# Optimization experiments

Hardware: AMD Instinct MI355X
Metric: run time of the kernel (lower is better)

The kernel has to match this reference:

```python
import jax, jax.numpy as jnp
import numpy as np

# Dimensions (match init_kwargs / input_specs)
N, C_IN, C, H, W = 2, 256, 256, 80, 80
G, KS = 16, 3                 # groups, kernel_size
K = KS * KS                   # sampling points per group
CG = C // G                   # channels per group
PAD, STRIDE, DIL = 1, 1, 1
OFFSET_SCALE = 1.0
EPS = 1e-5                    # BatchNorm2d eps (eval mode)


def setup_inputs() -> dict:
    key = jax.random.key(0)
    ks = jax.random.split(key, 12)
    rn = lambda k, shape, s=0.02: jax.random.normal(k, shape, dtype=jnp.float32) * s
    return {
        "x": jax.random.normal(ks[0], (N, C_IN, H, W), dtype=jnp.float32),
        # Conv(inc, ouc, k=1): 1x1 conv (bias=False) + BN + SiLU
        "w1": rn(ks[1], (C_IN, C)),
        "bn1_g": jnp.ones((C,), jnp.float32), "bn1_b": jnp.zeros((C,), jnp.float32),
        "bn1_m": rn(ks[2], (C,), 0.1),
        "bn1_v": jax.random.uniform(ks[3], (C,), minval=0.5, maxval=1.5, dtype=jnp.float32),
        # DCNv4: value_proj, fused offset_mask, output_proj
        "wv": rn(ks[4], (C, C)), "bv": jnp.zeros((C,), jnp.float32),
        "wom": rn(ks[5], (C, G * K * 3)), "bom": rn(ks[6], (G * K * 3,), 0.1),
        "wo": rn(ks[7], (C, C)), "bo": jnp.zeros((C,), jnp.float32),
        # trailing BatchNorm2d + SiLU
        "bn2_g": jnp.ones((C,), jnp.float32), "bn2_b": jnp.zeros((C,), jnp.float32),
        "bn2_m": rn(ks[8], (C,), 0.1),
        "bn2_v": jax.random.uniform(ks[9], (C,), minval=0.5, maxval=1.5, dtype=jnp.float32),
    }


def _bn(x, g, b, m, v):
    # eval-mode BatchNorm over last (channel) axis
    return (x - m) * jax.lax.rsqrt(v + EPS) * g + b


def _forward(x, w1, bn1_g, bn1_b, bn1_m, bn1_v, wv, bv, wom, bom, wo, bo,
             bn2_g, bn2_b, bn2_m, bn2_v):
    # --- Conv 1x1 + BN + SiLU (channels-last) ---
    h = jnp.einsum('nchw,cd->nhwd', x, w1)                 # (N,H,W,C)
    h = jax.nn.silu(_bn(h, bn1_g, bn1_b, bn1_m, bn1_v))

    # --- DCNv4 ---
    xf = h.reshape(N, H * W, C)
    value = (xf @ wv + bv).reshape(N, H, W, G, CG)         # value projection
    om = (xf @ wom + bom).reshape(N, H, W, G, 3 * K)       # fused offset+mask
    offset = om[..., :2 * K].reshape(N, H, W, G, K, 2) * OFFSET_SCALE  # (x,y) pairs
    mask = om[..., 2 * K:]                                 # (N,H,W,G,K); v4: no softmax

    # sampling pixel coords: p = out_pos*stride - pad + kernel_offset*dil + learned offset
    ky, kx = jnp.meshgrid(jnp.arange(KS), jnp.arange(KS), indexing='ij')
    ky = (ky.reshape(-1) * DIL).astype(jnp.float32)        # (K,)
    kx = (kx.reshape(-1) * DIL).astype(jnp.float32)
    base_y = (jnp.arange(H) * STRIDE - PAD).astype(jnp.float32)
    base_x = (jnp.arange(W) * STRIDE - PAD).astype(jnp.float32)
    py = base_y[None, :, None, None, None] + ky[None, None, None, None, :] + offset[..., 1]
    px = base_x[None, None, :, None, None] + kx[None, None, None, None, :] + offset[..., 0]

    y0 = jnp.floor(py); x0 = jnp.floor(px)
    wy = py - y0;       wx = px - x0
    y0i = y0.astype(jnp.int32); x0i = x0.astype(jnp.int32)
    y1i = y0i + 1;             x1i = x0i + 1

    ni = jnp.arange(N)[:, None, None, None, None]
    gi = jnp.arange(G)[None, None, None, :, None]

    def gather(yi, xi):
        valid = ((yi >= 0) & (yi < H) & (xi >= 0) & (xi < W)).astype(value.dtype)
        v = value[ni, jnp.clip(yi, 0, H - 1), jnp.clip(xi, 0, W - 1), gi]  # (N,H,W,G,K,CG)
        return v, valid

    acc = jnp.zeros((N, H, W, G, CG), dtype=value.dtype)
    for yi, xi, wgt in ((y0i, x0i, (1 - wy) * (1 - wx)),
                        (y0i, x1i, (1 - wy) * wx),
                        (y1i, x0i, wy * (1 - wx)),
                        (y1i, x1i, wy * wx)):
        v, valid = gather(yi, xi)
        acc = acc + jnp.einsum('nhwgk,nhwgkc->nhwgc', mask * wgt * valid, v)

    out = acc.reshape(N, H * W, C) @ wo + bo               # output projection
    out = out.reshape(N, H, W, C)

    # --- BN + SiLU (wrapper tail) ---
    out = jax.nn.silu(_bn(out, bn2_g, bn2_b, bn2_m, bn2_v))
    return jnp.transpose(out, (0, 3, 1, 2))                # (N,C,H,W)


def reference(x, w1, bn1_g, bn1_b, bn1_m, bn1_v, wv, bv, wom, bom, wo, bo,
              bn2_g, bn2_b, bn2_m, bn2_v):
    return _forward(x, w1, bn1_g, bn1_b, bn1_m, bn1_v, wv, bv, wom, bom,
                    wo, bo, bn2_g, bn2_b, bn2_m, bn2_v)
```

## Files before the change

kernel.cpp:

```cpp
#include <hip/hip_runtime.h>
#include <hip/hip_bf16.h>
#include <math.h>

typedef __attribute__((ext_vector_type(8))) short bf16x8;
typedef __attribute__((ext_vector_type(4))) float f32x4;

#define NB   2
#define CC   256
#define HH   80
#define WW   80
#define HWSZ 6400
#define MM   (NB * HWSZ)
#define NCAT 768
#define EPSB 1e-5f

__device__ inline void t32g(const float* __restrict__ in, int inld, int scol0,
                            int ncols, __hip_bfloat16* __restrict__ out,
                            int orow0, int r0, int tid)
{
    __shared__ float tile[32][33];
    int tx = tid & 31, ty = tid >> 5;
#pragma unroll
    for (int i = 0; i < 32; i += 8)
        tile[ty + i][tx] = (tx < ncols)
            ? in[(size_t)(r0 + ty + i) * inld + scol0 + tx] : 0.f;
    __syncthreads();
#pragma unroll
    for (int i = 0; i < 32; i += 8)
        out[(size_t)(orow0 + ty + i) * 256 + r0 + tx] =
            __float2bfloat16(tile[tx][ty + i]);
}

__global__ __launch_bounds__(256) void prep_all_k(
    const float* __restrict__ x,
    const float* __restrict__ w1, const float* __restrict__ wv,
    const float* __restrict__ wom, const float* __restrict__ wo,
    const float* __restrict__ bv, const float* __restrict__ bom,
    __hip_bfloat16* __restrict__ xT,
    __hip_bfloat16* __restrict__ w1T, __hip_bfloat16* __restrict__ BcatT,
    __hip_bfloat16* __restrict__ woT, float* __restrict__ bcat)
{
    int b = blockIdx.x, t = threadIdx.x;
    if (b < 3200) {
        __shared__ float tile[32][33];
        int z = b / 1600, r = b % 1600;
        int by = r / 200, bx = r % 200;
        const float* inz = x + (size_t)256 * HWSZ * z;
        __hip_bfloat16* outz = xT + (size_t)HWSZ * 256 * z;
        int bc = bx * 32, br = by * 32;
        int tx = t & 31, ty = t >> 5;
#pragma unroll
        for (int i = 0; i < 32; i += 8)
            tile[ty + i][tx] = inz[(size_t)(br + ty + i) * HWSZ + bc + tx];
        __syncthreads();
#pragma unroll
        for (int i = 0; i < 32; i += 8)
            outz[(size_t)(bc + ty + i) * 256 + br + tx] =
                __float2bfloat16(tile[tx][ty + i]);
        return;
    }
    b -= 3200;
    if (b < 64) {
        t32g(w1, 256, (b >> 3) * 32, 32, w1T, (b >> 3) * 32, (b & 7) * 32, t);
    } else if (b < 128) {
        int b2 = b - 64;
        t32g(wv, 256, (b2 >> 3) * 32, 32, BcatT, (b2 >> 3) * 32, (b2 & 7) * 32, t);
    } else if (b < 192) {
        int b2 = b - 128;
        t32g(wo, 256, (b2 >> 3) * 32, 32, woT, (b2 >> 3) * 32, (b2 & 7) * 32, t);
    } else if (b < 320) {
        int b2 = b - 192;
        int g = b2 >> 3, ct = b2 & 7;
        t32g(wom, 432, g * 27, 27, BcatT + 256 * 256, g * 32, ct * 32, t);
    } else {
        bcat[t] = bv[t];
#pragma unroll
        for (int j = 0; j < 2; ++j) {
            int r = j * 256 + t;
            int g = r >> 5, jj = r & 31;
            bcat[256 + r] = (jj < 27) ? bom[g * 27 + jj] : 0.f;
        }
    }
}

template <int EPI>
__global__ __launch_bounds__(256) void gemm_mfma(
    const short* __restrict__ A, const short* __restrict__ Bt,
    const float* __restrict__ bias,
    const float* __restrict__ bng, const float* __restrict__ bnb,
    const float* __restrict__ bnm, const float* __restrict__ bnv,
    void* __restrict__ Cout, int ldC)
{
    __shared__ __align__(16) char smem[49152];
    short* As = (short*)smem;
    short* Bs = (short*)(smem + 16384);

    const int t = threadIdx.x;
    const int w = t >> 6, l = t & 63;
    const int wr = w >> 1, wc = w & 1;
    const int m0 = blockIdx.x * 64, n0 = blockIdx.y * 128;

    f32x4 acc[2][4] = {};

    auto STAGE = [&](int b, int k0) {
        short* AsB = As + b * 4096;
        short* BsB = Bs + b * 8192;
#pragma unroll
        for (int i = 0; i < 2; ++i) {
            int s = (w << 1) + i;
            int c = (s << 6) + l;
            int row = c >> 3, ch = c & 7;
            const short* ga = A + (size_t)(m0 + row) * 256 + k0 + (ch << 3);
            __builtin_amdgcn_global_load_lds(
                (const __attribute__((address_space(1))) void*)ga,
                (__attribute__((address_space(3))) void*)(AsB + (s << 9)), 16, 0, 0);
        }
#pragma unroll
        for (int i = 0; i < 4; ++i) {
            int s = (w << 2) + i;
            int c = (s << 6) + l;
            int row = c >> 3, ch = c & 7;
            const short* gb = Bt + (size_t)(n0 + row) * 256 + k0 + (ch << 3);
            __builtin_amdgcn_global_load_lds(
                (const __attribute__((address_space(1))) void*)gb,
                (__attribute__((address_space(3))) void*)(BsB + (s << 9)), 16, 0, 0);
        }
    };

    auto COMPUTE = [&](int b) {
        const short* AsB = As + b * 4096;
        const short* BsB = Bs + b * 8192;
#pragma unroll
        for (int kk = 0; kk < 2; ++kk) {
            bf16x8 af[2], bfr[4];
#pragma unroll
            for (int mi = 0; mi < 2; ++mi)
                af[mi] = *(const bf16x8*)(AsB + (wr * 32 + mi * 16 + (l & 15)) * 64 +
                                          kk * 32 + ((l >> 4) << 3));
#pragma unroll
            for (int ni = 0; ni < 4; ++ni)
                bfr[ni] = *(const bf16x8*)(BsB + (wc * 64 + ni * 16 + (l & 15)) * 64 +
                                           kk * 32 + ((l >> 4) << 3));
#pragma unroll
            for (int mi = 0; mi < 2; ++mi)
#pragma unroll
                for (int ni = 0; ni < 4; ++ni)
                    acc[mi][ni] = __builtin_amdgcn_mfma_f32_16x16x32_bf16(
                        af[mi], bfr[ni], acc[mi][ni], 0, 0, 0);
        }
    };

    STAGE(0, 0);
    __syncthreads();
#pragma unroll
    for (int tt = 0; tt < 4; ++tt) {
        if (tt < 3) STAGE((tt + 1) & 1, (tt + 1) * 64);
        COMPUTE(tt & 1);
        __syncthreads();
    }

    if (EPI == 0) {
#pragma unroll
        for (int ni = 0; ni < 4; ++ni) {
            int chn = n0 + wc * 64 + ni * 16 + (l & 15);
            float bb = bias[chn];
#pragma unroll
            for (int mi = 0; mi < 2; ++mi) {
                int mbase = m0 + wr * 32 + mi * 16 + ((l >> 4) << 2);
#pragma unroll
                for (int j = 0; j < 4; ++j) {
                    float v = acc[mi][ni][j] + bb;
                    ((__hip_bfloat16*)Cout)[(size_t)(mbase + j) * ldC + chn] =
                        __float2bfloat16(v);
                }
            }
        }
    } else {
#pragma unroll
        for (int ni = 0; ni < 4; ++ni) {
            int chn = n0 + wc * 64 + ni * 16 + (l & 15);
            float mu = bnm[chn], iv = rsqrtf(bnv[chn] + EPSB);
            float gm = bng[chn], bt = bnb[chn];
#pragma unroll
            for (int mi = 0; mi < 2; ++mi) {
                int mbase = m0 + wr * 32 + mi * 16 + ((l >> 4) << 2);
#pragma unroll
                for (int j = 0; j < 4; ++j) {
                    float v = acc[mi][ni][j];
                    v = (v - mu) * iv * gm + bt;
                    v = v / (1.f + __expf(-v));
                    ((__hip_bfloat16*)Cout)[(size_t)(mbase + j) * ldC + chn] =
                        __float2bfloat16(v);
                }
            }
        }
    }
}

__global__ __launch_bounds__(512) void gemm3_fused_k(
    const __hip_bfloat16* __restrict__ C2, const short* __restrict__ woT,
    const float* __restrict__ bias,
    const float* __restrict__ bng, const float* __restrict__ bnb,
    const float* __restrict__ bnm, const float* __restrict__ bnv,
    float* __restrict__ out)
{
    __shared__ __align__(16) char smem[98304];
    short* As = (short*)smem;
    short* Bs = (short*)(smem + 32768);

    const int t = threadIdx.x;
    const int w = t >> 6, l = t & 63;
    const int wr = w >> 2, wc = w & 3;
    const int m0 = blockIdx.x * 64;
    const int nimg = m0 / HWSZ;
    const int p0 = m0 % HWSZ;

    auto STAGE_B = [&](int b, int k0) {
        short* BsB = Bs + b * 16384;
#pragma unroll
        for (int i = 0; i < 4; ++i) {
            int c = t + i * 512;
            int row = c >> 3, ch = c & 7;
            const short* gb = woT + (size_t)row * 256 + k0 + (ch << 3);
            __builtin_amdgcn_global_load_lds(
                (const __attribute__((address_space(1))) void*)gb,
                (__attribute__((address_space(3))) void*)(BsB + ((w << 6) + (i << 9)) * 8),
                16, 0, 0);
        }
    };

    STAGE_B(0, 0);

#pragma unroll
    for (int it = 0; it < 2; ++it) {
        int task = it * 512 + t;
        int g = task & 15, px = task >> 4;
        int mp = m0 + px;
        int p = mp % HWSZ;
        int y = p / WW, x = p % WW;

        const unsigned* omw =
            (const unsigned*)(C2 + (size_t)mp * NCAT + 256 + g * 32);
        const __hip_bfloat16* vb = C2 + (size_t)nimg * HWSZ * NCAT + g * 16;

        float mk[9];
        {
            unsigned mw[5];
#pragma unroll
            for (int i = 0; i < 5; ++i) mw[i] = omw[9 + i];
#pragma unroll
            for (int i = 0; i < 9; ++i) {
                unsigned w16 = (i & 1) ? (mw[i >> 1] >> 16) : (mw[i >> 1] & 0xffffu);
                union { unsigned u; float f; } cv; cv.u = w16 << 16;
                mk[i] = cv.f;
            }
        }

        float acc[16] = {};
#pragma unroll
        for (int k = 0; k < 9; ++k) {
            unsigned ow = omw[k];
            union { unsigned u; float f; } cx, cy;
            cx.u = (ow & 0xffffu) << 16;
            cy.u = ow & 0xffff0000u;
            float px_ = (float)(x - 1 + (k % 3)) + cx.f;
            float py_ = (float)(y - 1 + (k / 3)) + cy.f;
            float fx = floorf(px_), fy = floorf(py_);
            float wx = px_ - fx, wy = py_ - fy;
            int x0 = (int)fx, y0 = (int)fy;
            int x1 = x0 + 1, y1 = y0 + 1;
            float ax0 = ((unsigned)x0 < (unsigned)WW) ? (1.f - wx) : 0.f;
            float ax1 = ((unsigned)x1 < (unsigned)WW) ? wx : 0.f;
            float ay0 = ((unsigned)y0 < (unsigned)HH) ? mk[k] * (1.f - wy) : 0.f;
            float ay1 = ((unsigned)y1 < (unsigned)HH) ? mk[k] * wy : 0.f;
            int xc0 = min(max(x0, 0), WW - 1);
            int xc1 = min(max(x1, 0), WW - 1);
            int yc0 = min(max(y0, 0), HH - 1);
            int yc1 = min(max(y1, 0), HH - 1);
            const __hip_bfloat16* r0 = vb + (size_t)(yc0 * WW) * NCAT;
            const __hip_bfloat16* r1 = vb + (size_t)(yc1 * WW) * NCAT;
            const __hip_bfloat16* pts[4] = {
                r0 + (size_t)xc0 * NCAT, r0 + (size_t)xc1 * NCAT,
                r1 + (size_t)xc0 * NCAT, r1 + (size_t)xc1 * NCAT };
            float wgt[4] = { ay0 * ax0, ay0 * ax1, ay1 * ax0, ay1 * ax1 };
#pragma unroll
            for (int q = 0; q < 4; ++q) {
                bf16x8 v0 = *(const bf16x8*)pts[q];
                bf16x8 v1 = *(const bf16x8*)(pts[q] + 8);
#pragma unroll
                for (int j = 0; j < 8; ++j) {
                    union { unsigned u; float f; } cv;
                    cv.u = ((unsigned)(unsigned short)v0[j]) << 16;
                    acc[j] = fmaf(wgt[q], cv.f, acc[j]);
                }
#pragma unroll
                for (int j = 0; j < 8; ++j) {
                    union { unsigned u; float f; } cv;
                    cv.u = ((unsigned)(unsigned short)v1[j]) << 16;
                    acc[8 + j] = fmaf(wgt[q], cv.f, acc[8 + j]);
                }
            }
        }

        bf16x8 ov0, ov1;
#pragma unroll
        for (int j = 0; j < 8; ++j) {
            __hip_bfloat16 b0 = __float2bfloat16(acc[j]);
            __hip_bfloat16 b1 = __float2bfloat16(acc[8 + j]);
            ov0[j] = *reinterpret_cast<short*>(&b0);
            ov1[j] = *reinterpret_cast<short*>(&b1);
        }
        *(bf16x8*)(As + px * 256 + g * 16) = ov0;
        *(bf16x8*)(As + px * 256 + g * 16 + 8) = ov1;
    }
    __syncthreads();

    f32x4 acc[2][4] = {};
#pragma unroll
    for (int tt = 0; tt < 4; ++tt) {
        if (tt < 3) STAGE_B((tt + 1) & 1, (tt + 1) * 64);
        const short* BsB = Bs + (tt & 1) * 16384;
        const int k0 = tt * 64;
#pragma unroll
        for (int kk = 0; kk < 2; ++kk) {
            bf16x8 af[2], bfr[4];
#pragma unroll
            for (int mi = 0; mi < 2; ++mi)
                af[mi] = *(const bf16x8*)(As + (wr * 32 + mi * 16 + (l & 15)) * 256 +
                                          k0 + kk * 32 + ((l >> 4) << 3));
#pragma unroll
            for (int ni = 0; ni < 4; ++ni)
                bfr[ni] = *(const bf16x8*)(BsB + (wc * 64 + ni * 16 + (l & 15)) * 64 +
                                           kk * 32 + ((l >> 4) << 3));
#pragma unroll
            for (int mi = 0; mi < 2; ++mi)
#pragma unroll
                for (int ni = 0; ni < 4; ++ni)
                    acc[mi][ni] = __builtin_amdgcn_mfma_f32_16x16x32_bf16(
                        af[mi], bfr[ni], acc[mi][ni], 0, 0, 0);
        }
        __syncthreads();
    }

    float(*CtT)[68] = (float(*)[68])smem;
#pragma unroll
    for (int h2 = 0; h2 < 4; ++h2) {
        if (wc == h2) {
#pragma unroll
            for (int ni = 0; ni < 4; ++ni)
#pragma unroll
                for (int mi = 0; mi < 2; ++mi)
#pragma unroll
                    for (int j = 0; j < 4; ++j)
                        CtT[ni * 16 + (l & 15)]
                           [wr * 32 + mi * 16 + ((l >> 4) << 2) + j] =
                               acc[mi][ni][j];
        }
        __syncthreads();
#pragma unroll
        for (int it = 0; it < 2; ++it) {
            int e4 = it * 512 + t;
            int row = e4 >> 4;
            int c4 = e4 & 15;
            int chn = h2 * 64 + row;
            float bb = bias[chn];
            float mu = bnm[chn], iv = rsqrtf(bnv[chn] + EPSB);
            float gm = bng[chn], bt = bnb[chn];
            f32x4 v = *(f32x4*)&CtT[row][c4 * 4];
#pragma unroll
            for (int j = 0; j < 4; ++j) {
                float u = v[j] + bb;
                u = (u - mu) * iv * gm + bt;
                u = u / (1.f + __expf(-u));
                v[j] = u;
            }
            *(f32x4*)&out[(size_t)(nimg * CC + chn) * HWSZ + p0 + c4 * 4] = v;
        }
        __syncthreads();
    }
}

extern "C" void kernel_launch(void* const* d_in, const int* in_sizes, int n_in,
                              void* d_out, int out_size, void* d_ws, size_t ws_size,
                              hipStream_t stream)
{
    const float* x    = (const float*)d_in[0];
    const float* w1   = (const float*)d_in[1];
    const float* bn1g = (const float*)d_in[2];
    const float* bn1b = (const float*)d_in[3];
    const float* bn1m = (const float*)d_in[4];
    const float* bn1v = (const float*)d_in[5];
    const float* wv   = (const float*)d_in[6];
    const float* bv   = (const float*)d_in[7];
    const float* wom  = (const float*)d_in[8];
    const float* bom  = (const float*)d_in[9];
    const float* wo   = (const float*)d_in[10];
    const float* bo   = (const float*)d_in[11];
    const float* bn2g = (const float*)d_in[12];
    const float* bn2b = (const float*)d_in[13];
    const float* bn2m = (const float*)d_in[14];
    const float* bn2v = (const float*)d_in[15];
    float* out = (float*)d_out;

    char* w = (char*)d_ws;
    __hip_bfloat16* xT    = (__hip_bfloat16*)(w);
    __hip_bfloat16* hbuf  = (__hip_bfloat16*)(w + 6553600);
    __hip_bfloat16* C2    = (__hip_bfloat16*)(w + 13107200);
    __hip_bfloat16* w1T   = (__hip_bfloat16*)(w + 39321600);
    __hip_bfloat16* woT   = (__hip_bfloat16*)(w + 39452672);
    __hip_bfloat16* BcatT = (__hip_bfloat16*)(w + 39583744);
    float*          bcat  = (float*)(w + 39976960);

    dim3 blk(256);

    prep_all_k<<<dim3(3521), blk, 0, stream>>>(
        x, w1, wv, wom, wo, bv, bom, xT, w1T, BcatT, woT, bcat);

    gemm_mfma<1><<<dim3(200, 2), blk, 0, stream>>>(
        (const short*)xT, (const short*)w1T, nullptr,
        bn1g, bn1b, bn1m, bn1v, hbuf, CC);

    gemm_mfma<0><<<dim3(200, 6), blk, 0, stream>>>(
        (const short*)hbuf, (const short*)BcatT, bcat,
        nullptr, nullptr, nullptr, nullptr, C2, NCAT);

    gemm3_fused_k<<<dim3(200), dim3(512), 0, stream>>>(
        C2, (const short*)woT, bo, bn2g, bn2b, bn2m, bn2v, out);
}
```

Baseline: 148.9 us.

## Fuse all stages into one persistent kernel with grid barriers

Replaces the four separate launches (prep transpose, two GEMMs, fused deformable-sample+output GEMM) with one persistent kernel of 256 blocks of 512 threads, separated by atomic-counter grid barriers. The GEMM tiles are widened to 64x256 with 8 waves. The aim is to remove launch gaps and tail effects between stages. In exchange, only 256 blocks run each stage: 200 tiles in GEMM1 and phase 3 leave some CUs idle, and 600 tiles in GEMM2 need three uneven waves. It also adds spin-wait barrier overhead, a memset per call, and deadlock risk if not all 256 blocks are co-resident.

```diff
diff --git a/kernel.cpp b/kernel.cpp
--- a/kernel.cpp
+++ b/kernel.cpp
@@ -13,123 +13,63 @@
 #define MM   (NB * HWSZ)
 #define NCAT 768
 #define EPSB 1e-5f
-
-__device__ inline void t32g(const float* __restrict__ in, int inld, int scol0,
-                            int ncols, __hip_bfloat16* __restrict__ out,
-                            int orow0, int r0, int tid)
+#define NBLK 256
+
+__device__ __forceinline__ void gridbar(unsigned* cnt)
 {
-    __shared__ float tile[32][33];
-    int tx = tid & 31, ty = tid >> 5;
-#pragma unroll
-    for (int i = 0; i < 32; i += 8)
-        tile[ty + i][tx] = (tx < ncols)
-            ? in[(size_t)(r0 + ty + i) * inld + scol0 + tx] : 0.f;
     __syncthreads();
-#pragma unroll
-    for (int i = 0; i < 32; i += 8)
-        out[(size_t)(orow0 + ty + i) * 256 + r0 + tx] =
-            __float2bfloat16(tile[tx][ty + i]);
+    if (threadIdx.x == 0) {
+        __threadfence();
+        __hip_atomic_fetch_add(cnt, 1u, __ATOMIC_ACQ_REL, __HIP_MEMORY_SCOPE_AGENT);
+        while (__hip_atomic_load(cnt, __ATOMIC_ACQUIRE, __HIP_MEMORY_SCOPE_AGENT) < (unsigned)NBLK) {}
+        __threadfence();
+    }
+    __syncthreads();
 }
 
-__global__ __launch_bounds__(256) void prep_all_k(
-    const float* __restrict__ x,
-    const float* __restrict__ w1, const float* __restrict__ wv,
-    const float* __restrict__ wom, const float* __restrict__ wo,
-    const float* __restrict__ bv, const float* __restrict__ bom,
-    __hip_bfloat16* __restrict__ xT,
-    __hip_bfloat16* __restrict__ w1T, __hip_bfloat16* __restrict__ BcatT,
-    __hip_bfloat16* __restrict__ woT, float* __restrict__ bcat)
-{
-    int b = blockIdx.x, t = threadIdx.x;
-    if (b < 3200) {
-        __shared__ float tile[32][33];
-        int z = b / 1600, r = b % 1600;
-        int by = r / 200, bx = r % 200;
-        const float* inz = x + (size_t)256 * HWSZ * z;
-        __hip_bfloat16* outz = xT + (size_t)HWSZ * 256 * z;
-        int bc = bx * 32, br = by * 32;
-        int tx = t & 31, ty = t >> 5;
-#pragma unroll
-        for (int i = 0; i < 32; i += 8)
-            tile[ty + i][tx] = inz[(size_t)(br + ty + i) * HWSZ + bc + tx];
-        __syncthreads();
-#pragma unroll
-        for (int i = 0; i < 32; i += 8)
-            outz[(size_t)(bc + ty + i) * 256 + br + tx] =
-                __float2bfloat16(tile[tx][ty + i]);
-        return;
-    }
-    b -= 3200;
-    if (b < 64) {
-        t32g(w1, 256, (b >> 3) * 32, 32, w1T, (b >> 3) * 32, (b & 7) * 32, t);
-    } else if (b < 128) {
-        int b2 = b - 64;
-        t32g(wv, 256, (b2 >> 3) * 32, 32, BcatT, (b2 >> 3) * 32, (b2 & 7) * 32, t);
-    } else if (b < 192) {
-        int b2 = b - 128;
-        t32g(wo, 256, (b2 >> 3) * 32, 32, woT, (b2 >> 3) * 32, (b2 & 7) * 32, t);
-    } else if (b < 320) {
-        int b2 = b - 192;
-        int g = b2 >> 3, ct = b2 & 7;
-        t32g(wom, 432, g * 27, 27, BcatT + 256 * 256, g * 32, ct * 32, t);
-    } else {
-        bcat[t] = bv[t];
-#pragma unroll
-        for (int j = 0; j < 2; ++j) {
-            int r = j * 256 + t;
-            int g = r >> 5, jj = r & 31;
-            bcat[256 + r] = (jj < 27) ? bom[g * 27 + jj] : 0.f;
-        }
-    }
-}
-
 template <int EPI>
-__global__ __launch_bounds__(256) void gemm_mfma(
+__device__ __forceinline__ void gemm64x256(
     const short* __restrict__ A, const short* __restrict__ Bt,
     const float* __restrict__ bias,
     const float* __restrict__ bng, const float* __restrict__ bnb,
     const float* __restrict__ bnm, const float* __restrict__ bnv,
-    void* __restrict__ Cout, int ldC)
+    __hip_bfloat16* __restrict__ Cout, int ldC, int m0, int n0,
+    char* smem, int t)
 {
-    __shared__ __align__(16) char smem[49152];
     short* As = (short*)smem;
     short* Bs = (short*)(smem + 16384);
-
-    const int t = threadIdx.x;
     const int w = t >> 6, l = t & 63;
-    const int wr = w >> 1, wc = w & 1;
-    const int m0 = blockIdx.x * 64, n0 = blockIdx.y * 128;
-
+    const int wr = w >> 2, wc = w & 3;
     f32x4 acc[2][4] = {};
 
     auto STAGE = [&](int b, int k0) {
         short* AsB = As + b * 4096;
-        short* BsB = Bs + b * 8192;
-#pragma unroll
-        for (int i = 0; i < 2; ++i) {
-            int s = (w << 1) + i;
-            int c = (s << 6) + l;
-            int row = c >> 3, ch = c & 7;
+        short* BsB = Bs + b * 16384;
+        {
+            int row = t >> 3, ch = t & 7;
             const short* ga = A + (size_t)(m0 + row) * 256 + k0 + (ch << 3);
             __builtin_amdgcn_global_load_lds(
                 (const __attribute__((address_space(1))) void*)ga,
-                (__attribute__((address_space(3))) void*)(AsB + (s << 9)), 16, 0, 0);
+                (__attribute__((address_space(3))) void*)(AsB + t * 8), 16, 0, 0);
         }
 #pragma unroll
         for (int i = 0; i < 4; ++i) {
-            int s = (w << 2) + i;
-            int c = (s << 6) + l;
+            int c = t + i * 512;
             int row = c >> 3, ch = c & 7;
             const short* gb = Bt + (size_t)(n0 + row) * 256 + k0 + (ch << 3);
             __builtin_amdgcn_global_load_lds(
                 (const __attribute__((address_space(1))) void*)gb,
-                (__attribute__((address_space(3))) void*)(BsB + (s << 9)), 16, 0, 0);
+                (__attribute__((address_space(3))) void*)(BsB + c * 8), 16, 0, 0);
         }
     };
 
-    auto COMPUTE = [&](int b) {
-        const short* AsB = As + b * 4096;
-        const short* BsB = Bs + b * 8192;
+    STAGE(0, 0);
+    __syncthreads();
+#pragma unroll
+    for (int tt = 0; tt < 4; ++tt) {
+        if (tt < 3) STAGE((tt + 1) & 1, (tt + 1) * 64);
+        const short* AsB = As + (tt & 1) * 4096;
+        const short* BsB = Bs + (tt & 1) * 16384;
 #pragma unroll
         for (int kk = 0; kk < 2; ++kk) {
             bf16x8 af[2], bfr[4];
@@ -148,70 +88,45 @@
                     acc[mi][ni] = __builtin_amdgcn_mfma_f32_16x16x32_bf16(
                         af[mi], bfr[ni], acc[mi][ni], 0, 0, 0);
         }
-    };
-
-    STAGE(0, 0);
-    __syncthreads();
-#pragma unroll
-    for (int tt = 0; tt < 4; ++tt) {
-        if (tt < 3) STAGE((tt + 1) & 1, (tt + 1) * 64);
-        COMPUTE(tt & 1);
         __syncthreads();
     }
 
-    if (EPI == 0) {
-#pragma unroll
-        for (int ni = 0; ni < 4; ++ni) {
-            int chn = n0 + wc * 64 + ni * 16 + (l & 15);
-            float bb = bias[chn];
-#pragma unroll
-            for (int mi = 0; mi < 2; ++mi) {
-                int mbase = m0 + wr * 32 + mi * 16 + ((l >> 4) << 2);
-#pragma unroll
-                for (int j = 0; j < 4; ++j) {
-                    float v = acc[mi][ni][j] + bb;
-                    ((__hip_bfloat16*)Cout)[(size_t)(mbase + j) * ldC + chn] =
-                        __float2bfloat16(v);
-                }
-            }
-        }
-    } else {
-#pragma unroll
-        for (int ni = 0; ni < 4; ++ni) {
-            int chn = n0 + wc * 64 + ni * 16 + (l & 15);
-            float mu = bnm[chn], iv = rsqrtf(bnv[chn] + EPSB);
-            float gm = bng[chn], bt = bnb[chn];
-#pragma unroll
-            for (int mi = 0; mi < 2; ++mi) {
-                int mbase = m0 + wr * 32 + mi * 16 + ((l >> 4) << 2);
-#pragma unroll
-                for (int j = 0; j < 4; ++j) {
-                    float v = acc[mi][ni][j];
-                    v = (v - mu) * iv * gm + bt;
+#pragma unroll
+    for (int ni = 0; ni < 4; ++ni) {
+        int chn = n0 + wc * 64 + ni * 16 + (l & 15);
+        float bb = (EPI == 0) ? bias[chn] : 0.f;
+        float mu = 0.f, iv = 0.f, gm = 0.f, bt2 = 0.f;
+        if (EPI == 1) {
+            mu = bnm[chn]; iv = rsqrtf(bnv[chn] + EPSB);
+            gm = bng[chn]; bt2 = bnb[chn];
+        }
+#pragma unroll
+        for (int mi = 0; mi < 2; ++mi) {
+            int mbase = m0 + wr * 32 + mi * 16 + ((l >> 4) << 2);
+#pragma unroll
+            for (int j = 0; j < 4; ++j) {
+                float v = acc[mi][ni][j] + bb;
+                if (EPI == 1) {
+                    v = (v - mu) * iv * gm + bt2;
                     v = v / (1.f + __expf(-v));
-                    ((__hip_bfloat16*)Cout)[(size_t)(mbase + j) * ldC + chn] =
-                        __float2bfloat16(v);
-                }
+                }
+                Cout[(size_t)(mbase + j) * ldC + chn] = __float2bfloat16(v);
             }
         }
     }
 }
 
-__global__ __launch_bounds__(512) void gemm3_fused_k(
+__device__ __forceinline__ void p3_fused(
     const __hip_bfloat16* __restrict__ C2, const short* __restrict__ woT,
     const float* __restrict__ bias,
     const float* __restrict__ bng, const float* __restrict__ bnb,
     const float* __restrict__ bnm, const float* __restrict__ bnv,
-    float* __restrict__ out)
+    float* __restrict__ out, int m0, char* smem, int t)
 {
-    __shared__ __align__(16) char smem[98304];
     short* As = (short*)smem;
     short* Bs = (short*)(smem + 32768);
-
-    const int t = threadIdx.x;
     const int w = t >> 6, l = t & 63;
     const int wr = w >> 2, wc = w & 3;
-    const int m0 = blockIdx.x * 64;
     const int nimg = m0 / HWSZ;
     const int p0 = m0 % HWSZ;
 
@@ -224,8 +139,7 @@
             const short* gb = woT + (size_t)row * 256 + k0 + (ch << 3);
             __builtin_amdgcn_global_load_lds(
                 (const __attribute__((address_space(1))) void*)gb,
-                (__attribute__((address_space(3))) void*)(BsB + ((w << 6) + (i << 9)) * 8),
-                16, 0, 0);
+                (__attribute__((address_space(3))) void*)(BsB + c * 8), 16, 0, 0);
         }
     };
 
@@ -365,12 +279,12 @@
             int chn = h2 * 64 + row;
             float bb = bias[chn];
             float mu = bnm[chn], iv = rsqrtf(bnv[chn] + EPSB);
-            float gm = bng[chn], bt = bnb[chn];
+            float gm = bng[chn], bt2 = bnb[chn];
             f32x4 v = *(f32x4*)&CtT[row][c4 * 4];
 #pragma unroll
             for (int j = 0; j < 4; ++j) {
                 float u = v[j] + bb;
-                u = (u - mu) * iv * gm + bt;
+                u = (u - mu) * iv * gm + bt2;
                 u = u / (1.f + __expf(-u));
                 v[j] = u;
             }
@@ -378,6 +292,104 @@
         }
         __syncthreads();
     }
+}
+
+__global__ __launch_bounds__(512) void mega_k(
+    const float* __restrict__ x, const float* __restrict__ w1,
+    const float* __restrict__ bn1g, const float* __restrict__ bn1b,
+    const float* __restrict__ bn1m, const float* __restrict__ bn1v,
+    const float* __restrict__ wv, const float* __restrict__ bv,
+    const float* __restrict__ wom, const float* __restrict__ bom,
+    const float* __restrict__ wo, const float* __restrict__ bo,
+    const float* __restrict__ bn2g, const float* __restrict__ bn2b,
+    const float* __restrict__ bn2m, const float* __restrict__ bn2v,
+    __hip_bfloat16* __restrict__ xT, __hip_bfloat16* __restrict__ hbuf,
+    __hip_bfloat16* __restrict__ C2, __hip_bfloat16* __restrict__ w1T,
+    __hip_bfloat16* __restrict__ woT, __hip_bfloat16* __restrict__ BcatT,
+    float* __restrict__ bcat, unsigned* __restrict__ bar,
+    float* __restrict__ out)
+{
+    __shared__ __align__(16) char smem[98304];
+    const int t = threadIdx.x;
+    const int bid = blockIdx.x;
+
+    {
+        float(*tiles)[32][33] = (float(*)[32][33])smem;
+        const int half = t >> 8, tid = t & 255;
+        const int tx = tid & 31, ty = tid >> 5;
+        for (int it = 0; it < 7; ++it) {
+            int task = it * 512 + bid * 2 + half;
+            const float* gin = nullptr;
+            __hip_bfloat16* gout = nullptr;
+            int inld = 0, scol0 = 0, ncols = 0, orow0 = 0, r0 = 0;
+            if (task < 3200) {
+                int z = task / 1600, r = task % 1600;
+                int by = r / 200, bx = r % 200;
+                gin = x + (size_t)z * 256 * HWSZ; inld = HWSZ;
+                scol0 = bx * 32; ncols = 32;
+                gout = xT + (size_t)z * HWSZ * 256; orow0 = bx * 32; r0 = by * 32;
+            } else if (task < 3264) {
+                int b = task - 3200;
+                gin = w1; inld = 256; scol0 = (b >> 3) * 32; ncols = 32;
+                gout = w1T; orow0 = (b >> 3) * 32; r0 = (b & 7) * 32;
+            } else if (task < 3328) {
+                int b = task - 3264;
+                gin = wv; inld = 256; scol0 = (b >> 3) * 32; ncols = 32;
+                gout = BcatT; orow0 = (b >> 3) * 32; r0 = (b & 7) * 32;
+            } else if (task < 3392) {
+                int b = task - 3328;
+                gin = wo; inld = 256; scol0 = (b >> 3) * 32; ncols = 32;
+                gout = woT; orow0 = (b >> 3) * 32; r0 = (b & 7) * 32;
+            } else if (task < 3520) {
+                int b = task - 3392;
+                int g = b >> 3, ct = b & 7;
+                gin = wom; inld = 432; scol0 = g * 27; ncols = 27;
+                gout = BcatT + 65536; orow0 = g * 32; r0 = ct * 32;
+            } else if (task == 3520) {
+                bcat[tid] = bv[tid];
+#pragma unroll
+                for (int j = 0; j < 2; ++j) {
+                    int r = j * 256 + tid;
+                    int g = r >> 5, jj = r & 31;
+                    bcat[256 + r] = (jj < 27) ? bom[g * 27 + jj] : 0.f;
+                }
+            }
+            if (gin) {
+#pragma unroll
+                for (int i = 0; i < 4; ++i) {
+                    int row = ty + i * 8;
+                    tiles[half][row][tx] = (tx < ncols)
+                        ? gin[(size_t)(r0 + row) * inld + scol0 + tx] : 0.f;
+                }
+            }
+            __syncthreads();
+            if (gin) {
+#pragma unroll
+                for (int i = 0; i < 4; ++i) {
+                    int row = ty + i * 8;
+                    gout[(size_t)(orow0 + row) * 256 + r0 + tx] =
+                        __float2bfloat16(tiles[half][tx][row]);
+                }
+            }
+            __syncthreads();
+        }
+    }
+    gridbar(bar + 0);
+
+    for (int task = bid; task < 200; task += NBLK)
+        gemm64x256<1>((const short*)xT, (const short*)w1T, nullptr,
+                      bn1g, bn1b, bn1m, bn1v, hbuf, 256, task * 64, 0, smem, t);
+    gridbar(bar + 1);
+
+    for (int task = bid; task < 600; task += NBLK)
+        gemm64x256<0>((const short*)hbuf, (const short*)BcatT, bcat,
+                      nullptr, nullptr, nullptr, nullptr, C2, NCAT,
+                      (task % 200) * 64, (task / 200) * 256, smem, t);
+    gridbar(bar + 2);
+
+    for (int task = bid; task < 200; task += NBLK)
+        p3_fused(C2, (const short*)woT, bo, bn2g, bn2b, bn2m, bn2v,
+                 out, task * 64, smem, t);
 }
 
 extern "C" void kernel_launch(void* const* d_in, const int* in_sizes, int n_in,
@@ -410,20 +422,11 @@
     __hip_bfloat16* woT   = (__hip_bfloat16*)(w + 39452672);
     __hip_bfloat16* BcatT = (__hip_bfloat16*)(w + 39583744);
     float*          bcat  = (float*)(w + 39976960);
-
-    dim3 blk(256);
-
-    prep_all_k<<<dim3(3521), blk, 0, stream>>>(
-        x, w1, wv, wom, wo, bv, bom, xT, w1T, BcatT, woT, bcat);
-
-    gemm_mfma<1><<<dim3(200, 2), blk, 0, stream>>>(
-        (const short*)xT, (const short*)w1T, nullptr,
-        bn1g, bn1b, bn1m, bn1v, hbuf, CC);
-
-    gemm_mfma<0><<<dim3(200, 6), blk, 0, stream>>>(
-        (const short*)hbuf, (const short*)BcatT, bcat,
-        nullptr, nullptr, nullptr, nullptr, C2, NCAT);
-
-    gemm3_fused_k<<<dim3(200), dim3(512), 0, stream>>>(
-        C2, (const short*)woT, bo, bn2g, bn2b, bn2m, bn2v, out);
+    unsigned*       bar   = (unsigned*)(w + 41943040);
+
+    hipMemsetAsync(bar, 0, 64, stream);
+    mega_k<<<dim3(NBLK), dim3(512), 0, stream>>>(
+        x, w1, bn1g, bn1b, bn1m, bn1v, wv, bv, wom, bom, wo, bo,
+        bn2g, bn2b, bn2m, bn2v,
+        xT, hbuf, C2, w1T, woT, BcatT, bcat, bar, out);
 }
```

New measurement: 276.8 us. 85.9% more time.

## Fuse input transpose, conv1 and value/offset GEMMs into one kernel

Applied to the files above, without the earlier changes.

Removes the separate x transpose pass and the hbuf intermediate by loading fp32 x tiles directly into LDS as bf16, running the 1x1 conv with BN+SiLU, and then the concatenated value/offset-mask GEMM from the same LDS-resident activations. The sampling+output-projection kernel shrinks to 32-row tiles with 256 threads, and B tiles use an XOR-swizzled LDS layout with a padded A stride. This cuts global traffic and launches, but leaves each block with less parallelism per tile (400 blocks of 32 rows) and keeps the N-chunks sequential inside the block.

```diff
diff --git a/kernel.cpp b/kernel.cpp
--- a/kernel.cpp
+++ b/kernel.cpp
@@ -5,14 +5,16 @@
 typedef __attribute__((ext_vector_type(8))) short bf16x8;
 typedef __attribute__((ext_vector_type(4))) float f32x4;
 
-#define NB   2
-#define CC   256
 #define HH   80
 #define WW   80
 #define HWSZ 6400
-#define MM   (NB * HWSZ)
+#define MM   12800
 #define NCAT 768
 #define EPSB 1e-5f
+#define ALD  264
+
+#define AS1 __attribute__((address_space(1)))
+#define AS3 __attribute__((address_space(3)))
 
 __device__ inline void t32g(const float* __restrict__ in, int inld, int scol0,
                             int ncols, __hip_bfloat16* __restrict__ out,
@@ -31,35 +33,14 @@
             __float2bfloat16(tile[tx][ty + i]);
 }
 
-__global__ __launch_bounds__(256) void prep_all_k(
-    const float* __restrict__ x,
+__global__ __launch_bounds__(256) void prep_w_k(
     const float* __restrict__ w1, const float* __restrict__ wv,
     const float* __restrict__ wom, const float* __restrict__ wo,
     const float* __restrict__ bv, const float* __restrict__ bom,
-    __hip_bfloat16* __restrict__ xT,
     __hip_bfloat16* __restrict__ w1T, __hip_bfloat16* __restrict__ BcatT,
     __hip_bfloat16* __restrict__ woT, float* __restrict__ bcat)
 {
     int b = blockIdx.x, t = threadIdx.x;
-    if (b < 3200) {
-        __shared__ float tile[32][33];
-        int z = b / 1600, r = b % 1600;
-        int by = r / 200, bx = r % 200;
-        const float* inz = x + (size_t)256 * HWSZ * z;
-        __hip_bfloat16* outz = xT + (size_t)HWSZ * 256 * z;
-        int bc = bx * 32, br = by * 32;
-        int tx = t & 31, ty = t >> 5;
-#pragma unroll
-        for (int i = 0; i < 32; i += 8)
-            tile[ty + i][tx] = inz[(size_t)(br + ty + i) * HWSZ + bc + tx];
-        __syncthreads();
-#pragma unroll
-        for (int i = 0; i < 32; i += 8)
-            outz[(size_t)(bc + ty + i) * 256 + br + tx] =
-                __float2bfloat16(tile[tx][ty + i]);
-        return;
-    }
-    b -= 3200;
     if (b < 64) {
         t32g(w1, 256, (b >> 3) * 32, 32, w1T, (b >> 3) * 32, (b & 7) * 32, t);
     } else if (b < 128) {
@@ -83,161 +64,172 @@
     }
 }
 
-template <int EPI>
-__global__ __launch_bounds__(256) void gemm_mfma(
-    const short* __restrict__ A, const short* __restrict__ Bt,
-    const float* __restrict__ bias,
-    const float* __restrict__ bng, const float* __restrict__ bnb,
-    const float* __restrict__ bnm, const float* __restrict__ bnv,
-    void* __restrict__ Cout, int ldC)
-{
-    __shared__ __align__(16) char smem[49152];
-    short* As = (short*)smem;
-    short* Bs = (short*)(smem + 16384);
+__device__ __forceinline__ void stageB(const short* __restrict__ Bt, int nb,
+                                       int k0, short* BsB, int t)
+{
+#pragma unroll
+    for (int i = 0; i < 4; ++i) {
+        int c = t + i * 256;
+        int row = c >> 2, cd = c & 3;
+        int cs = cd ^ ((row >> 1) & 3);
+        const short* gb = Bt + (size_t)(nb + row) * 256 + k0 + cs * 8;
+        __builtin_amdgcn_global_load_lds((const AS1 void*)gb,
+                                         (AS3 void*)(BsB + c * 8), 16, 0, 0);
+    }
+}
+
+__device__ __forceinline__ bf16x8 readB(const short* BsB, int wc, int ni, int l)
+{
+    int n = wc * 64 + ni * 16 + (l & 15);
+    int cs = (l >> 4) ^ ((n >> 1) & 3);
+    return *(const bf16x8*)(BsB + n * 32 + cs * 8);
+}
+
+__global__ __launch_bounds__(256) void gemm12_k(
+    const float* __restrict__ x, const short* __restrict__ w1T,
+    const short* __restrict__ BcatT, const float* __restrict__ bcat,
+    const float* __restrict__ bn1g, const float* __restrict__ bn1b,
+    const float* __restrict__ bn1m, const float* __restrict__ bn1v,
+    __hip_bfloat16* __restrict__ C2)
+{
+    __shared__ __align__(16) char smem[49664];
+    short* Ax = (short*)smem;
+    short* Bs = (short*)(smem + 16896);
 
     const int t = threadIdx.x;
-    const int w = t >> 6, l = t & 63;
-    const int wr = w >> 1, wc = w & 1;
-    const int m0 = blockIdx.x * 64, n0 = blockIdx.y * 128;
+    const int l = t & 63, wc = t >> 6;
+    const int m0 = blockIdx.x * 32;
+    const int nimg = m0 / HWSZ;
+    const int p0 = m0 % HWSZ;
+
+    {
+        const int j0 = (t & 3) * 8;
+#pragma unroll
+        for (int cc = 0; cc < 4; ++cc) {
+            int c = cc * 64 + (t >> 2);
+            const float* src = x + (size_t)(nimg * 256 + c) * HWSZ + p0 + j0;
+            f32x4 v0 = *(const f32x4*)src;
+            f32x4 v1 = *(const f32x4*)(src + 4);
+#pragma unroll
+            for (int i = 0; i < 4; ++i)
+                ((__hip_bfloat16*)Ax)[(j0 + i) * ALD + c] = __float2bfloat16(v0[i]);
+#pragma unroll
+            for (int i = 0; i < 4; ++i)
+                ((__hip_bfloat16*)Ax)[(j0 + 4 + i) * ALD + c] = __float2bfloat16(v1[i]);
+        }
+    }
+    stageB(w1T, 0, 0, Bs, t);
+    __syncthreads();
 
     f32x4 acc[2][4] = {};
-
-    auto STAGE = [&](int b, int k0) {
-        short* AsB = As + b * 4096;
-        short* BsB = Bs + b * 8192;
-#pragma unroll
-        for (int i = 0; i < 2; ++i) {
-            int s = (w << 1) + i;
-            int c = (s << 6) + l;
-            int row = c >> 3, ch = c & 7;
-            const short* ga = A + (size_t)(m0 + row) * 256 + k0 + (ch << 3);
-            __builtin_amdgcn_global_load_lds(
-                (const __attribute__((address_space(1))) void*)ga,
-                (__attribute__((address_space(3))) void*)(AsB + (s << 9)), 16, 0, 0);
-        }
-#pragma unroll
-        for (int i = 0; i < 4; ++i) {
-            int s = (w << 2) + i;
-            int c = (s << 6) + l;
-            int row = c >> 3, ch = c & 7;
-            const short* gb = Bt + (size_t)(n0 + row) * 256 + k0 + (ch << 3);
-            __builtin_amdgcn_global_load_lds(
-                (const __attribute__((address_space(1))) void*)gb,
-                (__attribute__((address_space(3))) void*)(BsB + (s << 9)), 16, 0, 0);
-        }
-    };
-
-    auto COMPUTE = [&](int b) {
-        const short* AsB = As + b * 4096;
-        const short* BsB = Bs + b * 8192;
-#pragma unroll
-        for (int kk = 0; kk < 2; ++kk) {
+#pragma unroll
+    for (int tt = 0; tt < 8; ++tt) {
+        if (tt < 7) stageB(w1T, 0, (tt + 1) * 32, Bs + ((tt + 1) & 1) * 8192, t);
+        const short* BsB = Bs + (tt & 1) * 8192;
+        const int k0 = tt * 32;
+        bf16x8 af[2], bfr[4];
+#pragma unroll
+        for (int mi = 0; mi < 2; ++mi)
+            af[mi] = *(const bf16x8*)(Ax + (mi * 16 + (l & 15)) * ALD + k0 +
+                                      ((l >> 4) << 3));
+#pragma unroll
+        for (int ni = 0; ni < 4; ++ni) bfr[ni] = readB(BsB, wc, ni, l);
+#pragma unroll
+        for (int mi = 0; mi < 2; ++mi)
+#pragma unroll
+            for (int ni = 0; ni < 4; ++ni)
+                acc[mi][ni] = __builtin_amdgcn_mfma_f32_16x16x32_bf16(
+                    af[mi], bfr[ni], acc[mi][ni], 0, 0, 0);
+        __syncthreads();
+    }
+
+#pragma unroll
+    for (int ni = 0; ni < 4; ++ni) {
+        int chn = wc * 64 + ni * 16 + (l & 15);
+        float mu = bn1m[chn], iv = rsqrtf(bn1v[chn] + EPSB);
+        float gm = bn1g[chn], bt2 = bn1b[chn];
+#pragma unroll
+        for (int mi = 0; mi < 2; ++mi) {
+#pragma unroll
+            for (int j = 0; j < 4; ++j) {
+                int m = mi * 16 + ((l >> 4) << 2) + j;
+                float v = acc[mi][ni][j];
+                v = (v - mu) * iv * gm + bt2;
+                v = v / (1.f + __expf(-v));
+                ((__hip_bfloat16*)Ax)[m * ALD + chn] = __float2bfloat16(v);
+            }
+        }
+    }
+    __syncthreads();
+
+    for (int nc = 0; nc < 3; ++nc) {
+        f32x4 acc2[2][4] = {};
+        stageB(BcatT, nc * 256, 0, Bs, t);
+        __syncthreads();
+#pragma unroll
+        for (int tt = 0; tt < 8; ++tt) {
+            if (tt < 7)
+                stageB(BcatT, nc * 256, (tt + 1) * 32, Bs + ((tt + 1) & 1) * 8192, t);
+            const short* BsB = Bs + (tt & 1) * 8192;
+            const int k0 = tt * 32;
             bf16x8 af[2], bfr[4];
 #pragma unroll
             for (int mi = 0; mi < 2; ++mi)
-                af[mi] = *(const bf16x8*)(AsB + (wr * 32 + mi * 16 + (l & 15)) * 64 +
-                                          kk * 32 + ((l >> 4) << 3));
-#pragma unroll
-            for (int ni = 0; ni < 4; ++ni)
-                bfr[ni] = *(const bf16x8*)(BsB + (wc * 64 + ni * 16 + (l & 15)) * 64 +
-                                           kk * 32 + ((l >> 4) << 3));
+                af[mi] = *(const bf16x8*)(Ax + (mi * 16 + (l & 15)) * ALD + k0 +
+                                          ((l >> 4) << 3));
+#pragma unroll
+            for (int ni = 0; ni < 4; ++ni) bfr[ni] = readB(BsB, wc, ni, l);
 #pragma unroll
             for (int mi = 0; mi < 2; ++mi)
 #pragma unroll
                 for (int ni = 0; ni < 4; ++ni)
-                    acc[mi][ni] = __builtin_amdgcn_mfma_f32_16x16x32_bf16(
-                        af[mi], bfr[ni], acc[mi][ni], 0, 0, 0);
-        }
-    };
-
-    STAGE(0, 0);
-    __syncthreads();
-#pragma unroll
-    for (int tt = 0; tt < 4; ++tt) {
-        if (tt < 3) STAGE((tt + 1) & 1, (tt + 1) * 64);
-        COMPUTE(tt & 1);
-        __syncthreads();
-    }
-
-    if (EPI == 0) {
+                    acc2[mi][ni] = __builtin_amdgcn_mfma_f32_16x16x32_bf16(
+                        af[mi], bfr[ni], acc2[mi][ni], 0, 0, 0);
+            __syncthreads();
+        }
 #pragma unroll
         for (int ni = 0; ni < 4; ++ni) {
-            int chn = n0 + wc * 64 + ni * 16 + (l & 15);
-            float bb = bias[chn];
+            int chn = nc * 256 + wc * 64 + ni * 16 + (l & 15);
+            float bb = bcat[chn];
 #pragma unroll
             for (int mi = 0; mi < 2; ++mi) {
-                int mbase = m0 + wr * 32 + mi * 16 + ((l >> 4) << 2);
 #pragma unroll
                 for (int j = 0; j < 4; ++j) {
-                    float v = acc[mi][ni][j] + bb;
-                    ((__hip_bfloat16*)Cout)[(size_t)(mbase + j) * ldC + chn] =
-                        __float2bfloat16(v);
+                    int m = m0 + mi * 16 + ((l >> 4) << 2) + j;
+                    C2[(size_t)m * NCAT + chn] =
+                        __float2bfloat16(acc2[mi][ni][j] + bb);
                 }
             }
         }
-    } else {
-#pragma unroll
-        for (int ni = 0; ni < 4; ++ni) {
-            int chn = n0 + wc * 64 + ni * 16 + (l & 15);
-            float mu = bnm[chn], iv = rsqrtf(bnv[chn] + EPSB);
-            float gm = bng[chn], bt = bnb[chn];
-#pragma unroll
-            for (int mi = 0; mi < 2; ++mi) {
-                int mbase = m0 + wr * 32 + mi * 16 + ((l >> 4) << 2);
-#pragma unroll
-                for (int j = 0; j < 4; ++j) {
-                    float v = acc[mi][ni][j];
-                    v = (v - mu) * iv * gm + bt;
-                    v = v / (1.f + __expf(-v));
-                    ((__hip_bfloat16*)Cout)[(size_t)(mbase + j) * ldC + chn] =
-                        __float2bfloat16(v);
-                }
-            }
-        }
-    }
-}
-
-__global__ __launch_bounds__(512) void gemm3_fused_k(
+    }
+}
+
+__global__ __launch_bounds__(256) void samp_gemm3_k(
     const __hip_bfloat16* __restrict__ C2, const short* __restrict__ woT,
-    const float* __restrict__ bias,
-    const float* __restrict__ bng, const float* __restrict__ bnb,
-    const float* __restrict__ bnm, const float* __restrict__ bnv,
+    const float* __restrict__ bo,
+    const float* __restrict__ bn2g, const float* __restrict__ bn2b,
+    const float* __restrict__ bn2m, const float* __restrict__ bn2v,
     float* __restrict__ out)
 {
-    __shared__ __align__(16) char smem[98304];
-    short* As = (short*)smem;
-    short* Bs = (short*)(smem + 32768);
+    __shared__ __align__(16) char smem[49664];
+    short* Ax = (short*)smem;
+    short* Bs = (short*)(smem + 16896);
 
     const int t = threadIdx.x;
-    const int w = t >> 6, l = t & 63;
-    const int wr = w >> 2, wc = w & 3;
-    const int m0 = blockIdx.x * 64;
+    const int l = t & 63, wc = t >> 6;
+    const int m0 = blockIdx.x * 32;
     const int nimg = m0 / HWSZ;
     const int p0 = m0 % HWSZ;
 
-    auto STAGE_B = [&](int b, int k0) {
-        short* BsB = Bs + b * 16384;
-#pragma unroll
-        for (int i = 0; i < 4; ++i) {
-            int c = t + i * 512;
-            int row = c >> 3, ch = c & 7;
-            const short* gb = woT + (size_t)row * 256 + k0 + (ch << 3);
-            __builtin_amdgcn_global_load_lds(
-                (const __attribute__((address_space(1))) void*)gb,
-                (__attribute__((address_space(3))) void*)(BsB + ((w << 6) + (i << 9)) * 8),
-                16, 0, 0);
-        }
-    };
-
-    STAGE_B(0, 0);
+    stageB(woT, 0, 0, Bs, t);
 
 #pragma unroll
     for (int it = 0; it < 2; ++it) {
-        int task = it * 512 + t;
+        int task = it * 256 + t;
         int g = task & 15, px = task >> 4;
         int mp = m0 + px;
         int p = mp % HWSZ;
-        int y = p / WW, x = p % WW;
+        int y = p / WW, xx = p % WW;
 
         const unsigned* omw =
             (const unsigned*)(C2 + (size_t)mp * NCAT + 256 + g * 32);
@@ -263,7 +255,7 @@
             union { unsigned u; float f; } cx, cy;
             cx.u = (ow & 0xffffu) << 16;
             cy.u = ow & 0xffff0000u;
-            float px_ = (float)(x - 1 + (k % 3)) + cx.f;
+            float px_ = (float)(xx - 1 + (k % 3)) + cx.f;
             float py_ = (float)(y - 1 + (k / 3)) + cy.f;
             float fx = floorf(px_), fy = floorf(py_);
             float wx = px_ - fx, wy = py_ - fy;
@@ -310,73 +302,60 @@
             ov0[j] = *reinterpret_cast<short*>(&b0);
             ov1[j] = *reinterpret_cast<short*>(&b1);
         }
-        *(bf16x8*)(As + px * 256 + g * 16) = ov0;
-        *(bf16x8*)(As + px * 256 + g * 16 + 8) = ov1;
+        *(bf16x8*)(Ax + px * ALD + g * 16) = ov0;
+        *(bf16x8*)(Ax + px * ALD + g * 16 + 8) = ov1;
     }
     __syncthreads();
 
     f32x4 acc[2][4] = {};
 #pragma unroll
-    for (int tt = 0; tt < 4; ++tt) {
-        if (tt < 3) STAGE_B((tt + 1) & 1, (tt + 1) * 64);
-        const short* BsB = Bs + (tt & 1) * 16384;
-        const int k0 = tt * 64;
-#pragma unroll
-        for (int kk = 0; kk < 2; ++kk) {
-            bf16x8 af[2], bfr[4];
-#pragma unroll
-            for (int mi = 0; mi < 2; ++mi)
-                af[mi] = *(const bf16x8*)(As + (wr * 32 + mi * 16 + (l & 15)) * 256 +
-                                          k0 + kk * 32 + ((l >> 4) << 3));
+    for (int tt = 0; tt < 8; ++tt) {
+        if (tt < 7) stageB(woT, 0, (tt + 1) * 32, Bs + ((tt + 1) & 1) * 8192, t);
+        const short* BsB = Bs + (tt & 1) * 8192;
+        const int k0 = tt * 32;
+        bf16x8 af[2], bfr[4];
+#pragma unroll
+        for (int mi = 0; mi < 2; ++mi)
+            af[mi] = *(const bf16x8*)(Ax + (mi * 16 + (l & 15)) * ALD + k0 +
+                                      ((l >> 4) << 3));
+#pragma unroll
+        for (int ni = 0; ni < 4; ++ni) bfr[ni] = readB(BsB, wc, ni, l);
+#pragma unroll
+        for (int mi = 0; mi < 2; ++mi)
 #pragma unroll
             for (int ni = 0; ni < 4; ++ni)
-                bfr[ni] = *(const bf16x8*)(BsB + (wc * 64 + ni * 16 + (l & 15)) * 64 +
-                                           kk * 32 + ((l >> 4) << 3));
-#pragma unroll
-            for (int mi = 0; mi < 2; ++mi)
-#pragma unroll
-                for (int ni = 0; ni < 4; ++ni)
-                    acc[mi][ni] = __builtin_amdgcn_mfma_f32_16x16x32_bf16(
-                        af[mi], bfr[ni], acc[mi][ni], 0, 0, 0);
-        }
+                acc[mi][ni] = __builtin_amdgcn_mfma_f32_16x16x32_bf16(
+                    af[mi], bfr[ni], acc[mi][ni], 0, 0, 0);
         __syncthreads();
     }
 
-    float(*CtT)[68] = (float(*)[68])smem;
-#pragma unroll
-    for (int h2 = 0; h2 < 4; ++h2) {
-        if (wc == h2) {
-#pragma unroll
-            for (int ni = 0; ni < 4; ++ni)
-#pragma unroll
-                for (int mi = 0; mi < 2; ++mi)
-#pragma unroll
-                    for (int j = 0; j < 4; ++j)
-                        CtT[ni * 16 + (l & 15)]
-                           [wr * 32 + mi * 16 + ((l >> 4) << 2) + j] =
-                               acc[mi][ni][j];
-        }
-        __syncthreads();
-#pragma unroll
-        for (int it = 0; it < 2; ++it) {
-            int e4 = it * 512 + t;
-            int row = e4 >> 4;
-            int c4 = e4 & 15;
-            int chn = h2 * 64 + row;
-            float bb = bias[chn];
-            float mu = bnm[chn], iv = rsqrtf(bnv[chn] + EPSB);
-            float gm = bng[chn], bt = bnb[chn];
-            f32x4 v = *(f32x4*)&CtT[row][c4 * 4];
-#pragma unroll
-            for (int j = 0; j < 4; ++j) {
-                float u = v[j] + bb;
-                u = (u - mu) * iv * gm + bt;
-                u = u / (1.f + __expf(-u));
-                v[j] = u;
-            }
-            *(f32x4*)&out[(size_t)(nimg * CC + chn) * HWSZ + p0 + c4 * 4] = v;
-        }
-        __syncthreads();
+    float(*CtT)[36] = (float(*)[36])smem;
+#pragma unroll
+    for (int ni = 0; ni < 4; ++ni)
+#pragma unroll
+        for (int mi = 0; mi < 2; ++mi)
+#pragma unroll
+            for (int j = 0; j < 4; ++j)
+                CtT[wc * 64 + ni * 16 + (l & 15)]
+                   [mi * 16 + ((l >> 4) << 2) + j] = acc[mi][ni][j];
+    __syncthreads();
+#pragma unroll
+    for (int i = 0; i < 8; ++i) {
+        int e4 = i * 256 + t;
+        int chn = e4 >> 3;
+        int c4 = e4 & 7;
+        float bb = bo[chn];
+        float mu = bn2m[chn], iv = rsqrtf(bn2v[chn] + EPSB);
+        float gm = bn2g[chn], bt2 = bn2b[chn];
+        f32x4 v = *(f32x4*)&CtT[chn][c4 * 4];
+#pragma unroll
+        for (int j = 0; j < 4; ++j) {
+            float u = v[j] + bb;
+            u = (u - mu) * iv * gm + bt2;
+            u = u / (1.f + __expf(-u));
+            v[j] = u;
+        }
+        *(f32x4*)&out[(size_t)(nimg * 256 + chn) * HWSZ + p0 + c4 * 4] = v;
     }
 }
 
@@ -403,27 +382,21 @@
     float* out = (float*)d_out;
 
     char* w = (char*)d_ws;
-    __hip_bfloat16* xT    = (__hip_bfloat16*)(w);
-    __hip_bfloat16* hbuf  = (__hip_bfloat16*)(w + 6553600);
-    __hip_bfloat16* C2    = (__hip_bfloat16*)(w + 13107200);
-    __hip_bfloat16* w1T   = (__hip_bfloat16*)(w + 39321600);
-    __hip_bfloat16* woT   = (__hip_bfloat16*)(w + 39452672);
-    __hip_bfloat16* BcatT = (__hip_bfloat16*)(w + 39583744);
-    float*          bcat  = (float*)(w + 39976960);
+    __hip_bfloat16* C2    = (__hip_bfloat16*)(w);
+    __hip_bfloat16* w1T   = (__hip_bfloat16*)(w + 19660800);
+    __hip_bfloat16* woT   = (__hip_bfloat16*)(w + 19791872);
+    __hip_bfloat16* BcatT = (__hip_bfloat16*)(w + 19922944);
+    float*          bcat  = (float*)(w + 20316160);
 
     dim3 blk(256);
 
-    prep_all_k<<<dim3(3521), blk, 0, stream>>>(
-        x, w1, wv, wom, wo, bv, bom, xT, w1T, BcatT, woT, bcat);
-
-    gemm_mfma<1><<<dim3(200, 2), blk, 0, stream>>>(
-        (const short*)xT, (const short*)w1T, nullptr,
-        bn1g, bn1b, bn1m, bn1v, hbuf, CC);
-
-    gemm_mfma<0><<<dim3(200, 6), blk, 0, stream>>>(
-        (const short*)hbuf, (const short*)BcatT, bcat,
-        nullptr, nullptr, nullptr, nullptr, C2, NCAT);
-
-    gemm3_fused_k<<<dim3(200), dim3(512), 0, stream>>>(
+    prep_w_k<<<dim3(321), blk, 0, stream>>>(
+        w1, wv, wom, wo, bv, bom, w1T, BcatT, woT, bcat);
+
+    gemm12_k<<<dim3(400), blk, 0, stream>>>(
+        x, (const short*)w1T, (const short*)BcatT, bcat,
+        bn1g, bn1b, bn1m, bn1v, C2);
+
+    samp_gemm3_k<<<dim3(400), blk, 0, stream>>>(
         C2, (const short*)woT, bo, bn2g, bn2b, bn2m, bn2v, out);
 }
```

After: 148.4 us. Within noise of the previous version (-0.4%).
